# Optimization experiments

Measured on AMD Instinct MI355X. Metric: run time of the kernel, lower is better.

The kernel has to match this reference:

```python
import jax, jax.numpy as jnp
import numpy as np

H = 16  # heads
D = 1024  # hidden
HD = D // H
FF = 4096
EPS = 1e-12


def _linear_params(key, d_in, d_out):
    k1, k2 = jax.random.split(key)
    bound = 1.0 / np.sqrt(d_in)
    W = jax.random.uniform(k1, (d_in, d_out), minval=-bound, maxval=bound, dtype=jnp.float32)
    b = jax.random.uniform(k2, (d_out,), minval=-bound, maxval=bound, dtype=jnp.float32)
    return W, b


def setup_inputs() -> dict:
    key = jax.random.key(0)
    ks = jax.random.split(key, 8)
    x = jax.random.normal(ks[0], (4, 2048, D), dtype=jnp.float32)
    mask = jnp.ones((4, 1, 1, 2048), dtype=jnp.int32)
    Wq, bq = _linear_params(ks[1], D, D)
    Wk, bk = _linear_params(ks[2], D, D)
    Wv, bv = _linear_params(ks[3], D, D)
    Wo, bo = _linear_params(ks[4], D, D)
    W1, b1 = _linear_params(ks[5], D, FF)
    W2, b2 = _linear_params(ks[6], FF, D)
    g1 = jnp.ones((D,), jnp.float32); be1 = jnp.zeros((D,), jnp.float32)
    g2 = jnp.ones((D,), jnp.float32); be2 = jnp.zeros((D,), jnp.float32)
    return {"x": x, "mask": mask,
            "Wq": Wq, "bq": bq, "Wk": Wk, "bk": bk, "Wv": Wv, "bv": bv,
            "Wo": Wo, "bo": bo, "W1": W1, "b1": b1, "W2": W2, "b2": b2,
            "g1": g1, "be1": be1, "g2": g2, "be2": be2}


def _layernorm(x, g, b):
    mu = jnp.mean(x, axis=-1, keepdims=True)
    var = jnp.mean(jnp.square(x - mu), axis=-1, keepdims=True)
    return (x - mu) / jnp.sqrt(var + EPS) * g + b


def reference(x, mask, Wq, bq, Wk, bk, Wv, bv, Wo, bo, W1, b1, W2, b2, g1, be1, g2, be2):
    B, L, _ = x.shape
    h = _layernorm(x, g1, be1)
    # [B, H, L, HD]
    q = (h @ Wq + bq).reshape(B, L, H, HD).transpose(0, 2, 1, 3)
    k = (h @ Wk + bk).reshape(B, L, H, HD).transpose(0, 2, 1, 3)
    v = (h @ Wv + bv).reshape(B, L, H, HD).transpose(0, 2, 1, 3)
    scores = jnp.einsum('bhqd,bhkd->bhqk', q, k) / np.sqrt(HD).astype(np.float32)
    scores = jnp.where(mask == 0, jnp.float32(-1e9), scores)
    attn = jax.nn.softmax(scores, axis=-1)  # dropout = identity (eval mode)
    out = jnp.einsum('bhqk,bhkd->bhqd', attn, v)
    out = out.transpose(0, 2, 1, 3).reshape(B, L, D)
    x = x + (out @ Wo + bo)
    h = _layernorm(x, g2, be2)
    ff = jax.nn.gelu(h @ W1 + b1, approximate=False) @ W2 + b2
    return x + ff
```

## Files before the change

kernel.cpp:

```cpp
#include <hip/hip_runtime.h>
#include <stdint.h>

#define D_MODEL 1024
#define NHEAD   16
#define HDIM    64
#define FFDIM   4096
#define BATCH   4
#define SEQ     2048
#define ROWS    (BATCH*SEQ)

typedef unsigned short u16;
typedef __bf16 bf16_t;
typedef bf16_t bf16x8 __attribute__((ext_vector_type(8)));
typedef float  f32x4  __attribute__((ext_vector_type(4)));
typedef float  f32x16 __attribute__((ext_vector_type(16)));

#define SCQ 0.18033688011112042f

__device__ __forceinline__ u16 f2bf(float f) {
  union { float f; unsigned u; } v; v.f = f;
  unsigned r = v.u + 0x7fffu + ((v.u >> 16) & 1u);
  return (u16)(r >> 16);
}

__device__ __forceinline__ void gl2lds16(const void* g, void* l) {
  __builtin_amdgcn_global_load_lds((const __attribute__((address_space(1))) void*)g,
                                   (__attribute__((address_space(3))) void*)l, 16, 0, 0);
}

#define MFMA_BF16(a, b, c) __builtin_amdgcn_mfma_f32_16x16x32_bf16((a), (b), (c), 0, 0, 0)
#define MFMA32(a, b, c)    __builtin_amdgcn_mfma_f32_32x32x16_bf16((a), (b), (c), 0, 0, 0)
#define EXP2(x) __builtin_amdgcn_exp2f(x)

__device__ __forceinline__ bf16x8 mk8(unsigned a, unsigned b, unsigned c, unsigned d) {
  union { unsigned u[4]; bf16x8 v; } t;
  t.u[0] = a; t.u[1] = b; t.u[2] = c; t.u[3] = d;
  return t.v;
}

__global__ __launch_bounds__(256) void ln_kernel(const float* __restrict__ x,
                                                 const float* __restrict__ g,
                                                 const float* __restrict__ be,
                                                 u16* __restrict__ out) {
  __shared__ float red[10];
  int row = blockIdx.x;
  int t = threadIdx.x;
  const float* xr = x + (size_t)row * D_MODEL;
  float4 xv = ((const float4*)xr)[t];
  float s  = xv.x + xv.y + xv.z + xv.w;
  float s2 = xv.x*xv.x + xv.y*xv.y + xv.z*xv.z + xv.w*xv.w;
  for (int d = 32; d > 0; d >>= 1) { s += __shfl_down(s, d); s2 += __shfl_down(s2, d); }
  int wid = t >> 6;
  if ((t & 63) == 0) { red[wid*2] = s; red[wid*2+1] = s2; }
  __syncthreads();
  if (t == 0) {
    float a = 0.f, b2 = 0.f;
    for (int i = 0; i < 4; ++i) { a += red[i*2]; b2 += red[i*2+1]; }
    red[8] = a; red[9] = b2;
  }
  __syncthreads();
  float mu  = red[8] * (1.0f / D_MODEL);
  float var = red[9] * (1.0f / D_MODEL) - mu*mu;
  float rstd = rsqrtf(var + 1e-12f);
  float4 gv = ((const float4*)g)[t];
  float4 bv = ((const float4*)be)[t];
  unsigned long long o =
      (unsigned long long)f2bf((xv.x - mu) * rstd * gv.x + bv.x)
    | ((unsigned long long)f2bf((xv.y - mu) * rstd * gv.y + bv.y) << 16)
    | ((unsigned long long)f2bf((xv.z - mu) * rstd * gv.z + bv.z) << 32)
    | ((unsigned long long)f2bf((xv.w - mu) * rstd * gv.w + bv.w) << 48);
  ((unsigned long long*)out)[(size_t)row * (D_MODEL/4) + t] = o;
}

__global__ __launch_bounds__(256) void wt_kernel(const float* __restrict__ W,
                                                 u16* __restrict__ Wt, int K, int N) {
  __shared__ float tile[32][33];
  int n0 = blockIdx.x * 32, k0 = blockIdx.y * 32;
  int tx = threadIdx.x & 31, ty = threadIdx.x >> 5;
  #pragma unroll
  for (int i = 0; i < 4; ++i) {
    int k = ty + i*8;
    tile[k][tx] = W[(size_t)(k0 + k) * N + n0 + tx];
  }
  __syncthreads();
  #pragma unroll
  for (int i = 0; i < 4; ++i) {
    int n = ty + i*8;
    Wt[(size_t)(n0 + n) * K + k0 + tx] = f2bf(tile[tx][n]);
  }
}

__global__ __launch_bounds__(256) void vtrans_kernel(const u16* __restrict__ vb,
                                                     u16* __restrict__ vt) {
  __shared__ __align__(16) u16 tile[64][80];
  int kb = blockIdx.x * 64;
  int bh = blockIdx.y;
  int b = bh >> 4, h = bh & 15;
  int t = threadIdx.x;
  int key = t >> 2, dq = (t & 3) * 16;
  const u16* src = vb + (size_t)b*SEQ*D_MODEL + (size_t)(kb+key)*D_MODEL + h*HDIM + dq;
  *(bf16x8*)&tile[key][dq]     = *(const bf16x8*)(src);
  *(bf16x8*)&tile[key][dq + 8] = *(const bf16x8*)(src + 8);
  __syncthreads();
  int w = t >> 6, lane = t & 63;
  int kq = w * 16;
  u16 vals[16];
  #pragma unroll
  for (int e = 0; e < 16; ++e) vals[e] = tile[kq + e][lane];
  u16* dst = vt + (size_t)bh * HDIM * SEQ + (size_t)lane * SEQ + kb + kq;
  *(bf16x8*)dst       = *(const bf16x8*)&vals[0];
  *(bf16x8*)(dst + 8) = *(const bf16x8*)&vals[8];
}

__device__ __forceinline__ float gelu_f(float v) {
  return 0.5f * v * (1.0f + erff(v * 0.70710678118654752f));
}

template<int EPI>
__global__ __launch_bounds__(512, 4) void gemm256(const u16* __restrict__ A,
                                                  const u16* __restrict__ Bt,
                                                  const float* __restrict__ bias,
                                                  const float* __restrict__ resid,
                                                  void* __restrict__ outp,
                                                  int M, int N, int K,
                                                  const float* __restrict__ bias2,
                                                  const float* __restrict__ bias3,
                                                  void* __restrict__ out2,
                                                  void* __restrict__ out3) {
  __shared__ __align__(16) u16 sA[3][128*32];
  __shared__ __align__(16) u16 sB[3][256*32];
  const int tid = threadIdx.x;
  const int lane = tid & 63, w = tid >> 6;
  const int r = lane & 15, kg = lane >> 4;
  const int rs = (r >> 1) & 3;
  const int wr = w >> 2, wc = w & 3;

  const int gx = gridDim.x;
  const int nwg = gx * gridDim.y;
  const int orig = blockIdx.y * gx + blockIdx.x;
  const int lid = (orig & 7) * (nwg >> 3) + (orig >> 3);
  const int bm = lid / gx, bn = lid % gx;

  const int NT = K >> 5;

  size_t offA, offB[2];
  {
    int row = tid >> 2, g = tid & 3;
    offA = (size_t)(bm*128 + row) * K + ((g ^ ((row >> 1) & 3)) * 8);
  }
  #pragma unroll
  for (int u = 0; u < 2; ++u) {
    int slot = u*512 + tid;
    int row = slot >> 2, g = slot & 3;
    offB[u] = (size_t)(bn*256 + row) * K + ((g ^ ((row >> 1) & 3)) * 8);
  }

  f32x4 acc[4][4];
  #pragma unroll
  for (int m = 0; m < 4; ++m)
    #pragma unroll
    for (int n = 0; n < 4; ++n) acc[m][n] = f32x4{0.f, 0.f, 0.f, 0.f};

  const float* bsel = bias;
  u16* osel = (u16*)outp;
  int bnl = bn;
  float qscale = 1.0f;
  if (EPI == 3) {
    int sec = bn >> 2;
    bsel = (sec == 0) ? bias : (sec == 1 ? bias2 : bias3);
    osel = (u16*)((sec == 0) ? outp : (sec == 1 ? out2 : out3));
    if (sec == 0) qscale = SCQ;
    bnl = bn & 3;
  }
  float bv4[4];
  #pragma unroll
  for (int n = 0; n < 4; ++n) bv4[n] = bsel[bnl*256 + wc*64 + n*16 + r];

  auto stage = [&](int bbuf, int t) {
    const size_t koff = (size_t)t * 32;
    gl2lds16(A  + offA    + koff, &sA[bbuf][tid*8]);
    gl2lds16(Bt + offB[0] + koff, &sB[bbuf][tid*8]);
    gl2lds16(Bt + offB[1] + koff, &sB[bbuf][(512+tid)*8]);
  };

  stage(0, 0);
  stage(1, 1);
  asm volatile("s_waitcnt vmcnt(3)" ::: "memory");
  __builtin_amdgcn_s_barrier();

  int buf = 0;
  for (int t = 0; t < NT; ++t) {
    const bool pre = (t + 2 < NT);
    int nb = buf + 2; if (nb >= 3) nb -= 3;

    if (pre) stage(nb, t + 2);

    bf16x8 af[4], bfr[4];
    #pragma unroll
    for (int m = 0; m < 4; ++m)
      af[m]  = *(const bf16x8*)&sA[buf][(wr*64 + m*16 + r)*32 + ((kg ^ rs) * 8)];
    #pragma unroll
    for (int n = 0; n < 4; ++n)
      bfr[n] = *(const bf16x8*)&sB[buf][(wc*64 + n*16 + r)*32 + ((kg ^ rs) * 8)];

    asm volatile("s_waitcnt lgkmcnt(0)" ::: "memory");
    __builtin_amdgcn_sched_barrier(0);
    __builtin_amdgcn_s_setprio(1);
    #pragma unroll
    for (int m = 0; m < 4; ++m)
      #pragma unroll
      for (int n = 0; n < 4; ++n)
        acc[m][n] = MFMA_BF16(af[m], bfr[n], acc[m][n]);
    __builtin_amdgcn_s_setprio(0);

    if (pre) asm volatile("s_waitcnt vmcnt(3)" ::: "memory");
    else     asm volatile("s_waitcnt vmcnt(0)" ::: "memory");
    __builtin_amdgcn_s_barrier();
    buf += 1; if (buf >= 3) buf -= 3;
  }

  const int orow = bm*128 + wr*64;
  const int ocol = (EPI == 3 ? bnl : bn)*256 + wc*64;
  const int ostride = (EPI == 3) ? 1024 : N;
  #pragma unroll
  for (int m = 0; m < 4; ++m) {
    #pragma unroll
    for (int n = 0; n < 4; ++n) {
      #pragma unroll
      for (int j = 0; j < 4; ++j) {
        int rr = orow + m*16 + kg*4 + j;
        int cc = ocol + n*16 + r;
        size_t idx = (size_t)rr * ostride + cc;
        float v = acc[m][n][j] + bv4[n];
        if (EPI == 0)       ((u16*)outp)[idx]   = f2bf(v);
        else if (EPI == 1)  ((float*)outp)[idx] = resid[idx] + v;
        else if (EPI == 2)  ((u16*)outp)[idx]   = f2bf(gelu_f(v));
        else                osel[idx]           = f2bf(v * qscale);
      }
    }
  }
}

__global__ __launch_bounds__(256, 4) void attn_kernel(const u16* __restrict__ qb,
                                                      const u16* __restrict__ kb,
                                                      const u16* __restrict__ vt,
                                                      const int* __restrict__ mask,
                                                      u16* __restrict__ ob) {
  __shared__ __align__(16) u16 sK[2][64*64];
  __shared__ __align__(16) u16 sV[2][64*64];
  __shared__ float sAl[4][32];
  __shared__ unsigned char sOkPart[256];
  __shared__ unsigned sTileOk;
  const float THR2 = 11.541560327111708f;
  int tid = threadIdx.x;
  int lane = tid & 63, w = tid >> 6;
  int l31 = lane & 31, hi = lane >> 5;
  int qt = blockIdx.x;
  int bh = blockIdx.y;
  int b = bh >> 4, h = bh & 15;
  size_t qkbase = (size_t)b * SEQ * D_MODEL + (size_t)h * HDIM;
  const u16* vtb = vt + (size_t)bh * HDIM * SEQ;
  const int* mrow = mask + b * SEQ;

  {
    int ok = 1;
    #pragma unroll
    for (int e = 0; e < 8; ++e) ok &= (mrow[tid*8 + e] != 0);
    sOkPart[tid] = (unsigned char)ok;
  }
  __syncthreads();
  if (w == 0) {
    int a = 0;
    if (lane < 32) {
      a = 1;
      #pragma unroll
      for (int e = 0; e < 8; ++e) a &= sOkPart[lane*8 + e];
    }
    unsigned long long bits = __ballot(a != 0);
    if (lane == 0) sTileOk = (unsigned)(bits & 0xffffffffu);
  }
  __syncthreads();
  const unsigned tileOkBits = sTileOk;

  const u16* qrow = qb + qkbase + (size_t)(qt*128 + w*32 + l31) * D_MODEL + hi*8;
  bf16x8 qf[4];
  #pragma unroll
  for (int dstep = 0; dstep < 4; ++dstep)
    qf[dstep] = *(const bf16x8*)(qrow + dstep*16);

  f32x16 oacc0, oacc1;
  #pragma unroll
  for (int e = 0; e < 16; ++e) { oacc0[e] = 0.f; oacc1[e] = 0.f; }
  float m_run = -1e30f;
  float lsum  = 0.f;

  int ch0 = w*64 + lane, ch1 = ch0 + 256;
  int row0 = ch0 >> 3, col0 = ((ch0 & 7) ^ (row0 & 7)) * 8;
  int row1 = ch1 >> 3, col1 = ((ch1 & 7) ^ (row1 & 7)) * 8;
  const u16* kp0 = kb + qkbase + (size_t)row0 * D_MODEL + col0;
  const u16* kp1 = kb + qkbase + (size_t)row1 * D_MODEL + col1;
  const u16* vp0 = vtb + (size_t)row0 * SEQ + col0;
  const u16* vp1 = vtb + (size_t)row1 * SEQ + col1;

  const int NT = SEQ / 64;

  gl2lds16(kp0, &sK[0][ch0*8]);
  gl2lds16(kp1, &sK[0][ch1*8]);
  gl2lds16(vp0, &sV[0][ch0*8]);
  gl2lds16(vp1, &sV[0][ch1*8]);
  kp0 += 64*D_MODEL; kp1 += 64*D_MODEL; vp0 += 64; vp1 += 64;

  for (int kt = 0; kt < NT; ++kt) {
    int cur = kt & 1;
    int key0 = kt * 64;
    if (kt + 1 < NT) {
      gl2lds16(kp0, &sK[cur^1][ch0*8]);
      gl2lds16(kp1, &sK[cur^1][ch1*8]);
      gl2lds16(vp0, &sV[cur^1][ch0*8]);
      gl2lds16(vp1, &sV[cur^1][ch1*8]);
      kp0 += 64*D_MODEL; kp1 += 64*D_MODEL; vp0 += 64; vp1 += 64;
      asm volatile("s_waitcnt vmcnt(4)" ::: "memory");
    } else {
      asm volatile("s_waitcnt vmcnt(0)" ::: "memory");
    }
    __builtin_amdgcn_s_barrier();

    const u16* Kt = sK[cur];
    const u16* Vt = sV[cur];

    f32x16 s0, s1;
    #pragma unroll
    for (int e = 0; e < 16; ++e) { s0[e] = 0.f; s1[e] = 0.f; }
    #pragma unroll
    for (int dstep = 0; dstep < 4; ++dstep) {
      int g = dstep*2 + hi;
      bf16x8 kf0 = *(const bf16x8*)&Kt[l31*64        + ((g ^ (l31 & 7)) * 8)];
      bf16x8 kf1 = *(const bf16x8*)&Kt[(32 + l31)*64 + ((g ^ ((32 + l31) & 7)) * 8)];
      s0 = MFMA32(kf0, qf[dstep], s0);
      s1 = MFMA32(kf1, qf[dstep], s1);
    }

    if (!((tileOkBits >> kt) & 1u)) {
      #pragma unroll
      for (int reg = 0; reg < 16; ++reg) {
        int kr = (reg & 3) + 8*(reg >> 2) + 4*hi;
        if (!mrow[key0 + kr])      s0[reg] = -1e9f;
        if (!mrow[key0 + 32 + kr]) s1[reg] = -1e9f;
      }
    }

    float tm = s0[0];
    #pragma unroll
    for (int e = 1; e < 16; ++e) tm = fmaxf(tm, s0[e]);
    #pragma unroll
    for (int e = 0; e < 16; ++e) tm = fmaxf(tm, s1[e]);
    tm = fmaxf(tm, __shfl_xor(tm, 32));

    if (__any(tm > m_run + THR2)) {
      float mn = fmaxf(m_run, tm);
      float al = EXP2(m_run - mn);
      m_run = mn;
      lsum *= al;
      if (lane < 32) sAl[w][lane] = al;
      asm volatile("s_waitcnt lgkmcnt(0)" ::: "memory");
      #pragma unroll
      for (int reg = 0; reg < 16; ++reg) {
        float a2 = sAl[w][(reg & 3) + 8*(reg >> 2) + 4*hi];
        oacc0[reg] *= a2; oacc1[reg] *= a2;
      }
    }

    #pragma unroll
    for (int e = 0; e < 16; ++e) {
      s0[e] = EXP2(s0[e] - m_run); lsum += s0[e];
      s1[e] = EXP2(s1[e] - m_run); lsum += s1[e];
    }

    unsigned wa, wb, wc, wd, we, wf, wg, wh;
#define CVTPK(dst, lo_, hi_) asm("v_cvt_pk_bf16_f32 %0, %1, %2" : "=v"(dst) : "v"(lo_), "v"(hi_))
    CVTPK(wa, s0[0],  s0[1]);  CVTPK(wb, s0[2],  s0[3]);
    CVTPK(wc, s0[4],  s0[5]);  CVTPK(wd, s0[6],  s0[7]);
    CVTPK(we, s0[8],  s0[9]);  CVTPK(wf, s0[10], s0[11]);
    CVTPK(wg, s0[12], s0[13]); CVTPK(wh, s0[14], s0[15]);
    asm volatile("v_permlane32_swap_b32 %0, %1" : "+v"(wc), "+v"(wa));
    asm volatile("v_permlane32_swap_b32 %0, %1" : "+v"(wd), "+v"(wb));
    asm volatile("v_permlane32_swap_b32 %0, %1" : "+v"(wg), "+v"(we));
    asm volatile("v_permlane32_swap_b32 %0, %1" : "+v"(wh), "+v"(wf));
    bf16x8 pa0 = mk8(wa, wb, wc, wd);
    bf16x8 pa1 = mk8(we, wf, wg, wh);
    CVTPK(wa, s1[0],  s1[1]);  CVTPK(wb, s1[2],  s1[3]);
    CVTPK(wc, s1[4],  s1[5]);  CVTPK(wd, s1[6],  s1[7]);
    CVTPK(we, s1[8],  s1[9]);  CVTPK(wf, s1[10], s1[11]);
    CVTPK(wg, s1[12], s1[13]); CVTPK(wh, s1[14], s1[15]);
    asm volatile("v_permlane32_swap_b32 %0, %1" : "+v"(wc), "+v"(wa));
    asm volatile("v_permlane32_swap_b32 %0, %1" : "+v"(wd), "+v"(wb));
    asm volatile("v_permlane32_swap_b32 %0, %1" : "+v"(wg), "+v"(we));
    asm volatile("v_permlane32_swap_b32 %0, %1" : "+v"(wh), "+v"(wf));
    bf16x8 pa2 = mk8(wa, wb, wc, wd);
    bf16x8 pa3 = mk8(we, wf, wg, wh);
#undef CVTPK

    int r0 = l31, r1 = 32 + l31;
    #pragma unroll
    for (int kstep = 0; kstep < 4; ++kstep) {
      int g = kstep*2 + hi;
      bf16x8 vf0 = *(const bf16x8*)&Vt[r0*64 + ((g ^ (r0 & 7)) * 8)];
      bf16x8 vf1 = *(const bf16x8*)&Vt[r1*64 + ((g ^ (r1 & 7)) * 8)];
      bf16x8 pk = (kstep == 0) ? pa0 : (kstep == 1) ? pa1 : (kstep == 2) ? pa2 : pa3;
      oacc0 = MFMA32(pk, vf0, oacc0);
      oacc1 = MFMA32(pk, vf1, oacc1);
    }
    __builtin_amdgcn_s_barrier();
  }

  float lsumT = lsum + __shfl_xor(lsum, 32);
  if (lane < 32) sAl[w][lane] = 1.0f / lsumT;
  asm volatile("s_waitcnt lgkmcnt(0)" ::: "memory");
  #pragma unroll
  for (int reg = 0; reg < 16; ++reg) {
    int qr = (reg & 3) + 8*(reg >> 2) + 4*hi;
    float rc = sAl[w][qr];
    int qg = qt*128 + w*32 + qr;
    size_t base2 = (size_t)(b*SEQ + qg) * D_MODEL + h*HDIM + l31;
    ob[base2]      = f2bf(oacc0[reg] * rc);
    ob[base2 + 32] = f2bf(oacc1[reg] * rc);
  }
}

extern "C" void kernel_launch(void* const* d_in, const int* in_sizes, int n_in,
                              void* d_out, int out_size, void* d_ws, size_t ws_size,
                              hipStream_t stream) {
  const float* x   = (const float*)d_in[0];
  const int*  mask = (const int*)d_in[1];
  const float* Wq = (const float*)d_in[2];  const float* bq = (const float*)d_in[3];
  const float* Wk = (const float*)d_in[4];  const float* bk = (const float*)d_in[5];
  const float* Wv = (const float*)d_in[6];  const float* bv = (const float*)d_in[7];
  const float* Wo = (const float*)d_in[8];  const float* bo = (const float*)d_in[9];
  const float* W1 = (const float*)d_in[10]; const float* b1 = (const float*)d_in[11];
  const float* W2 = (const float*)d_in[12]; const float* b2 = (const float*)d_in[13];
  const float* g1 = (const float*)d_in[14]; const float* be1 = (const float*)d_in[15];
  const float* g2 = (const float*)d_in[16]; const float* be2 = (const float*)d_in[17];

  const size_t MB = 1u << 20;
  char* ws = (char*)d_ws;
  u16*  hln  = (u16*)(ws);
  u16*  vt   = (u16*)(ws);
  u16*  qb   = (u16*)(ws + 16*MB);
  u16*  kb   = (u16*)(ws + 32*MB);
  u16*  vb   = (u16*)(ws + 48*MB);
  u16*  attn = (u16*)(ws + 64*MB);
  u16*  ff1  = (u16*)(ws + 16*MB);
  float* x2  = (float*)(ws + 80*MB);
  u16*  WqkvT= (u16*)(ws + 112*MB);
  u16*  WqT  = WqkvT;
  u16*  WkT  = (u16*)(ws + 114*MB);
  u16*  WvT  = (u16*)(ws + 116*MB);
  u16*  WoT  = (u16*)(ws + 118*MB);
  u16*  W1T  = (u16*)(ws + 120*MB);
  u16*  W2T  = (u16*)(ws + 128*MB);

  dim3 tb(256);
  wt_kernel<<<dim3(1024/32, 1024/32), tb, 0, stream>>>(Wq, WqT, 1024, 1024);
  wt_kernel<<<dim3(1024/32, 1024/32), tb, 0, stream>>>(Wk, WkT, 1024, 1024);
  wt_kernel<<<dim3(1024/32, 1024/32), tb, 0, stream>>>(Wv, WvT, 1024, 1024);
  wt_kernel<<<dim3(1024/32, 1024/32), tb, 0, stream>>>(Wo, WoT, 1024, 1024);
  wt_kernel<<<dim3(4096/32, 1024/32), tb, 0, stream>>>(W1, W1T, 1024, 4096);
  wt_kernel<<<dim3(1024/32, 4096/32), tb, 0, stream>>>(W2, W2T, 4096, 1024);

  ln_kernel<<<ROWS, tb, 0, stream>>>(x, g1, be1, hln);

  dim3 gb(512);
  gemm256<3><<<dim3(3072/256, ROWS/128), gb, 0, stream>>>(hln, WqkvT, bq, nullptr, qb,
                                                          ROWS, 3072, 1024,
                                                          bk, bv, kb, vb);

  vtrans_kernel<<<dim3(SEQ/64, BATCH*NHEAD), tb, 0, stream>>>(vb, vt);

  attn_kernel<<<dim3(SEQ/128, BATCH*NHEAD), tb, 0, stream>>>(qb, kb, vt, mask, attn);

  gemm256<1><<<dim3(1024/256, ROWS/128), gb, 0, stream>>>(attn, WoT, bo, x, x2,
                                                          ROWS, 1024, 1024,
                                                          nullptr, nullptr, nullptr, nullptr);

  ln_kernel<<<ROWS, tb, 0, stream>>>(x2, g2, be2, hln);

  gemm256<2><<<dim3(4096/256, ROWS/128), gb, 0, stream>>>(hln, W1T, b1, nullptr, ff1,
                                                          ROWS, 4096, 1024,
                                                          nullptr, nullptr, nullptr, nullptr);

  gemm256<1><<<dim3(1024/256, ROWS/128), gb, 0, stream>>>(ff1, W2T, b2, x2, (float*)d_out,
                                                          ROWS, 1024, 4096,
                                                          nullptr, nullptr, nullptr, nullptr);
}
```

Before: 444.4 us.

## Retile GEMM to 256x128 blocks with 4 waves of 128x64 per wave

The GEMM block tile changes from 128x256 with 8 waves to 256x128 with 4 waves. Each wave now computes a 128x64 tile, holding 32 accumulators and 8 A fragments, which doubles the MFMA work per LDS fragment load. The QKV section split and the launch grids are updated to match, and an extra barrier is inserted before the MFMA loop. The cost is higher register pressure per wave and fewer waves per block to hide latency.

```diff
diff --git a/kernel.cpp b/kernel.cpp
--- a/kernel.cpp
+++ b/kernel.cpp
@@ -117,7 +117,7 @@
 }
 
 template<int EPI>
-__global__ __launch_bounds__(512, 4) void gemm256(const u16* __restrict__ A,
+__global__ __launch_bounds__(256, 2) void gemm256(const u16* __restrict__ A,
                                                   const u16* __restrict__ Bt,
                                                   const float* __restrict__ bias,
                                                   const float* __restrict__ resid,
@@ -127,13 +127,13 @@
                                                   const float* __restrict__ bias3,
                                                   void* __restrict__ out2,
                                                   void* __restrict__ out3) {
-  __shared__ __align__(16) u16 sA[3][128*32];
-  __shared__ __align__(16) u16 sB[3][256*32];
+  __shared__ __align__(16) u16 sA[3][256*32];
+  __shared__ __align__(16) u16 sB[3][128*32];
   const int tid = threadIdx.x;
   const int lane = tid & 63, w = tid >> 6;
   const int r = lane & 15, kg = lane >> 4;
   const int rs = (r >> 1) & 3;
-  const int wr = w >> 2, wc = w & 3;
+  const int wm = w >> 1, wn = w & 1;
 
   const int gx = gridDim.x;
   const int nwg = gx * gridDim.y;
@@ -143,21 +143,23 @@
 
   const int NT = K >> 5;
 
-  size_t offA, offB[2];
-  {
-    int row = tid >> 2, g = tid & 3;
-    offA = (size_t)(bm*128 + row) * K + ((g ^ ((row >> 1) & 3)) * 8);
+  size_t offA[4], offB[2];
+  #pragma unroll
+  for (int u = 0; u < 4; ++u) {
+    int slot = u*256 + tid;
+    int row = slot >> 2, j = slot & 3;
+    offA[u] = (size_t)(bm*256 + row) * K + ((j ^ ((row >> 1) & 3)) * 8);
   }
   #pragma unroll
   for (int u = 0; u < 2; ++u) {
-    int slot = u*512 + tid;
-    int row = slot >> 2, g = slot & 3;
-    offB[u] = (size_t)(bn*256 + row) * K + ((g ^ ((row >> 1) & 3)) * 8);
-  }
-
-  f32x4 acc[4][4];
-  #pragma unroll
-  for (int m = 0; m < 4; ++m)
+    int slot = u*256 + tid;
+    int row = slot >> 2, j = slot & 3;
+    offB[u] = (size_t)(bn*128 + row) * K + ((j ^ ((row >> 1) & 3)) * 8);
+  }
+
+  f32x4 acc[8][4];
+  #pragma unroll
+  for (int m = 0; m < 8; ++m)
     #pragma unroll
     for (int n = 0; n < 4; ++n) acc[m][n] = f32x4{0.f, 0.f, 0.f, 0.f};
 
@@ -166,26 +168,29 @@
   int bnl = bn;
   float qscale = 1.0f;
   if (EPI == 3) {
-    int sec = bn >> 2;
+    int sec = bn >> 3;
     bsel = (sec == 0) ? bias : (sec == 1 ? bias2 : bias3);
     osel = (u16*)((sec == 0) ? outp : (sec == 1 ? out2 : out3));
     if (sec == 0) qscale = SCQ;
-    bnl = bn & 3;
+    bnl = bn & 7;
   }
   float bv4[4];
   #pragma unroll
-  for (int n = 0; n < 4; ++n) bv4[n] = bsel[bnl*256 + wc*64 + n*16 + r];
+  for (int n = 0; n < 4; ++n) bv4[n] = bsel[bnl*128 + wn*64 + n*16 + r];
 
   auto stage = [&](int bbuf, int t) {
     const size_t koff = (size_t)t * 32;
-    gl2lds16(A  + offA    + koff, &sA[bbuf][tid*8]);
-    gl2lds16(Bt + offB[0] + koff, &sB[bbuf][tid*8]);
-    gl2lds16(Bt + offB[1] + koff, &sB[bbuf][(512+tid)*8]);
+    #pragma unroll
+    for (int u = 0; u < 4; ++u)
+      gl2lds16(A + offA[u] + koff, &sA[bbuf][(u*256 + tid)*8]);
+    #pragma unroll
+    for (int u = 0; u < 2; ++u)
+      gl2lds16(Bt + offB[u] + koff, &sB[bbuf][(u*256 + tid)*8]);
   };
 
   stage(0, 0);
   stage(1, 1);
-  asm volatile("s_waitcnt vmcnt(3)" ::: "memory");
+  asm volatile("s_waitcnt vmcnt(6)" ::: "memory");
   __builtin_amdgcn_s_barrier();
 
   int buf = 0;
@@ -195,35 +200,36 @@
 
     if (pre) stage(nb, t + 2);
 
-    bf16x8 af[4], bfr[4];
-    #pragma unroll
-    for (int m = 0; m < 4; ++m)
-      af[m]  = *(const bf16x8*)&sA[buf][(wr*64 + m*16 + r)*32 + ((kg ^ rs) * 8)];
+    bf16x8 af[8], bfr[4];
+    #pragma unroll
+    for (int m = 0; m < 8; ++m)
+      af[m]  = *(const bf16x8*)&sA[buf][(wm*128 + m*16 + r)*32 + ((kg ^ rs) * 8)];
     #pragma unroll
     for (int n = 0; n < 4; ++n)
-      bfr[n] = *(const bf16x8*)&sB[buf][(wc*64 + n*16 + r)*32 + ((kg ^ rs) * 8)];
-
+      bfr[n] = *(const bf16x8*)&sB[buf][(wn*64 + n*16 + r)*32 + ((kg ^ rs) * 8)];
+
+    __builtin_amdgcn_s_barrier();
     asm volatile("s_waitcnt lgkmcnt(0)" ::: "memory");
     __builtin_amdgcn_sched_barrier(0);
     __builtin_amdgcn_s_setprio(1);
     #pragma unroll
-    for (int m = 0; m < 4; ++m)
+    for (int m = 0; m < 8; ++m)
       #pragma unroll
       for (int n = 0; n < 4; ++n)
         acc[m][n] = MFMA_BF16(af[m], bfr[n], acc[m][n]);
     __builtin_amdgcn_s_setprio(0);
 
-    if (pre) asm volatile("s_waitcnt vmcnt(3)" ::: "memory");
+    if (pre) asm volatile("s_waitcnt vmcnt(6)" ::: "memory");
     else     asm volatile("s_waitcnt vmcnt(0)" ::: "memory");
     __builtin_amdgcn_s_barrier();
     buf += 1; if (buf >= 3) buf -= 3;
   }
 
-  const int orow = bm*128 + wr*64;
-  const int ocol = (EPI == 3 ? bnl : bn)*256 + wc*64;
+  const int orow = bm*256 + wm*128;
+  const int ocol = (EPI == 3 ? bnl : bn)*128 + wn*64;
   const int ostride = (EPI == 3) ? 1024 : N;
   #pragma unroll
-  for (int m = 0; m < 4; ++m) {
+  for (int m = 0; m < 8; ++m) {
     #pragma unroll
     for (int n = 0; n < 4; ++n) {
       #pragma unroll
@@ -469,8 +475,7 @@
 
   ln_kernel<<<ROWS, tb, 0, stream>>>(x, g1, be1, hln);
 
-  dim3 gb(512);
-  gemm256<3><<<dim3(3072/256, ROWS/128), gb, 0, stream>>>(hln, WqkvT, bq, nullptr, qb,
+  gemm256<3><<<dim3(3072/128, ROWS/256), tb, 0, stream>>>(hln, WqkvT, bq, nullptr, qb,
                                                           ROWS, 3072, 1024,
                                                           bk, bv, kb, vb);
 
@@ -478,17 +483,17 @@
 
   attn_kernel<<<dim3(SEQ/128, BATCH*NHEAD), tb, 0, stream>>>(qb, kb, vt, mask, attn);
 
-  gemm256<1><<<dim3(1024/256, ROWS/128), gb, 0, stream>>>(attn, WoT, bo, x, x2,
+  gemm256<1><<<dim3(1024/128, ROWS/256), tb, 0, stream>>>(attn, WoT, bo, x, x2,
                                                           ROWS, 1024, 1024,
                                                           nullptr, nullptr, nullptr, nullptr);
 
   ln_kernel<<<ROWS, tb, 0, stream>>>(x2, g2, be2, hln);
 
-  gemm256<2><<<dim3(4096/256, ROWS/128), gb, 0, stream>>>(hln, W1T, b1, nullptr, ff1,
+  gemm256<2><<<dim3(4096/128, ROWS/256), tb, 0, stream>>>(hln, W1T, b1, nullptr, ff1,
                                                           ROWS, 4096, 1024,
                                                           nullptr, nullptr, nullptr, nullptr);
 
-  gemm256<1><<<dim3(1024/256, ROWS/128), gb, 0, stream>>>(ff1, W2T, b2, x2, (float*)d_out,
+  gemm256<1><<<dim3(1024/128, ROWS/256), tb, 0, stream>>>(ff1, W2T, b2, x2, (float*)d_out,
                                                           ROWS, 1024, 4096,
                                                           nullptr, nullptr, nullptr, nullptr);
 }
```

Measured after the change: 516.3 us (median of 5 runs). +16.2%, slower.
